# Optimization experiments

Hardware: AMD Instinct MI355X
Metric: run time of the kernel (lower is better)

The kernel has to match this reference:

```python
import jax, jax.numpy as jnp
import numpy as np

N_NODES = 100000
N_EDGES = 600000
VOCAB = 5000
NUM_GRAPHS = 2000
NUM_CLASSES = 10


def setup_inputs() -> dict:
    key = jax.random.key(0)
    ks = jax.random.split(key, 12)
    x = jax.random.randint(ks[0], (N_NODES,), 0, VOCAB, dtype=jnp.int32)
    edge_index = jax.random.randint(ks[1], (2, N_EDGES), 0, N_NODES, dtype=jnp.int32)
    batch = jnp.sort(jax.random.randint(ks[2], (N_NODES,), 0, NUM_GRAPHS, dtype=jnp.int32))
    emb = jax.random.normal(ks[3], (VOCAB, 64), dtype=jnp.float32) * 0.1
    W1 = jax.random.normal(ks[4], (64, 128), dtype=jnp.float32) * (1.0 / np.sqrt(64))
    b1 = jnp.zeros((128,), dtype=jnp.float32)
    W2 = jax.random.normal(ks[5], (128, 128), dtype=jnp.float32) * (1.0 / np.sqrt(128))
    b2 = jnp.zeros((128,), dtype=jnp.float32)
    Wlin = jax.random.normal(ks[6], (128, NUM_CLASSES), dtype=jnp.float32) * (1.0 / np.sqrt(128))
    blin = jnp.zeros((NUM_CLASSES,), dtype=jnp.float32)
    return {"x": x, "edge_index": edge_index, "batch": batch, "num_graphs": NUM_GRAPHS,
            "emb": emb, "W1": W1, "b1": b1, "W2": W2, "b2": b2, "Wlin": Wlin, "blin": blin}


def reference(x, edge_index, batch, num_graphs, emb, W1, b1, W2, b2, Wlin, blin):
    N = x.shape[0]
    loops = jnp.arange(N, dtype=edge_index.dtype)
    src = jnp.concatenate([edge_index[0], loops])  # message sources (j)
    dst = jnp.concatenate([edge_index[1], loops])  # aggregation targets (i)
    # GCN symmetric normalization with self-loops (PyG gcn_norm, source_to_target)
    deg = jax.ops.segment_sum(jnp.ones_like(dst, dtype=jnp.float32), dst, num_segments=N)
    dinv = jnp.where(deg > 0, jax.lax.rsqrt(deg), 0.0)
    norm = dinv[src] * dinv[dst]  # [E+N]

    def gcn(h, W, b):
        h = h @ W  # linear transform first (GCNConv order)
        msg = h[src] * norm[:, None]  # gather + scale, [E+N, F]
        return jax.ops.segment_sum(msg, dst, num_segments=N) + b

    h = emb[x]  # [N, 64]
    h = jax.nn.relu(gcn(h, W1, b1))
    h = jax.nn.relu(gcn(h, W2, b2))
    g = jax.ops.segment_max(h, batch, num_segments=num_graphs)  # global_max_pool
    return g @ Wlin + blin
```

## Files before the change

kernel.cpp:

```cpp
#include <hip/hip_runtime.h>
#include <hip/hip_bf16.h>
#include <hip/hip_fp16.h>


typedef _Float16 h8 __attribute__((ext_vector_type(8)));
typedef float f32x4 __attribute__((ext_vector_type(4)));

__global__ __launch_bounds__(256) void k_zero(int4* __restrict__ deg, int n4i,
                                              int4* __restrict__ pool, int p4i) {
    int t = blockIdx.x * 256 + threadIdx.x;
    int4 z = make_int4(0, 0, 0, 0);
    if (t < n4i) deg[t] = z;
    if (t < p4i) pool[t] = z;
}

__global__ __launch_bounds__(256) void k_degprep(const int* __restrict__ dst, int* __restrict__ deg, int E,
                                                 const float* __restrict__ emb, __half2* __restrict__ e16,
                                                 const float* __restrict__ W1, _Float16* __restrict__ W1T,
                                                 const float* __restrict__ W2, _Float16* __restrict__ W2T,
                                                 int nEmbF, int gE, int nCast) {
    int bid = blockIdx.x;
    if (bid < gE) {
        int e = bid * 256 + threadIdx.x;
        if (e < E) atomicAdd(&deg[dst[e]], 1);
    } else if (bid < gE + nCast) {
        int t = (bid - gE) * 256 + threadIdx.x;
        if (t * 4 < nEmbF) {
            float4 v = *(const float4*)&emb[t * 4];
            e16[t * 2] = __floats2half2_rn(v.x, v.y);
            e16[t * 2 + 1] = __floats2half2_rn(v.z, v.w);
        }
    } else if (bid < gE + nCast + 32) {
        int t = (bid - gE - nCast) * 256 + threadIdx.x;
        int c = t >> 6, k = t & 63;
        W1T[c * 64 + k] = (_Float16)W1[k * 128 + c];
    } else {
        int t = (bid - gE - nCast - 32) * 256 + threadIdx.x;
        if (t < 128 * 128) {
            int c = t >> 7, k = t & 127;
            W2T[c * 128 + k] = (_Float16)W2[k * 128 + c];
        }
    }
}

__global__ __launch_bounds__(256) void k_scan1(const int* __restrict__ deg, int* __restrict__ exc,
                                               int* __restrict__ bsums, float* __restrict__ dinv, int N) {
    __shared__ int s[256];
    int i = blockIdx.x * 256 + threadIdx.x;
    int v = (i < N) ? deg[i] : 0;
    if (i < N) dinv[i] = rsqrtf((float)(v + 1));
    s[threadIdx.x] = v;
    __syncthreads();
    for (int off = 1; off < 256; off <<= 1) {
        int t = (threadIdx.x >= (unsigned)off) ? s[threadIdx.x - off] : 0;
        __syncthreads();
        s[threadIdx.x] += t;
        __syncthreads();
    }
    if (i < N) exc[i] = s[threadIdx.x] - v;
    if (threadIdx.x == 255) bsums[blockIdx.x] = s[255];
}

__global__ __launch_bounds__(512) void k_scan2(int* __restrict__ bsums, int nb) {
    __shared__ int s[512];
    int i = threadIdx.x;
    int v = (i < nb) ? bsums[i] : 0;
    s[i] = v;
    __syncthreads();
    for (int off = 1; off < 512; off <<= 1) {
        int t = (i >= off) ? s[i - off] : 0;
        __syncthreads();
        s[i] += t;
        __syncthreads();
    }
    if (i < nb) bsums[i] = s[i] - v;
}

__global__ __launch_bounds__(256) void k_scan3(int* __restrict__ rowstart, int* __restrict__ cursor,
                                               const int* __restrict__ bsums, int N, int E) {
    int i = blockIdx.x * 256 + threadIdx.x;
    if (i < N) {
        int r = rowstart[i] + bsums[blockIdx.x];
        rowstart[i] = r;
        cursor[i] = r;
    }
    if (i == 0 && blockIdx.x == 0) rowstart[N] = E;
}

__global__ __launch_bounds__(256) void k_fill(const int* __restrict__ src, const int* __restrict__ dst,
                                              const int* __restrict__ x, const float* __restrict__ dinv,
                                              int* __restrict__ cursor, int2* __restrict__ ed,
                                              int* __restrict__ cols, int E) {
    int e = blockIdx.x * 256 + threadIdx.x;
    if (e < E) {
        int d = dst[e];
        int s = src[e];
        int pos = atomicAdd(&cursor[d], 1);
        ed[pos] = make_int2(x[s], __float_as_int(dinv[s]));
        cols[pos] = s;
    }
}

__global__ __launch_bounds__(256) void k_agge(const __half2* __restrict__ e16, const int* __restrict__ x,
                                              const float* __restrict__ dinv, const int* __restrict__ rs,
                                              const int2* __restrict__ ed, __half2* __restrict__ Xagg, int N) {
    int lane = threadIdx.x & 31;
    int n0 = (blockIdx.x * 8 + (threadIdx.x >> 5)) * 2;
    if (n0 >= N) return;
    int nB = (n0 + 1 < N) ? n0 + 1 : n0;
    int cA0 = rs[n0], cA1 = rs[n0 + 1];
    int cB0 = rs[nB], cB1 = rs[nB + 1];
    bool hasA = cA0 < cA1, hasB = cB0 < cB1;
    __half2 tA[8], tB[8];
    float wA[8], wB[8];
    if (hasA) {
#pragma unroll
        for (int i = 0; i < 8; ++i) {
            int ei = cA0 + i;
            int ec = (ei < cA1) ? ei : cA1 - 1;
            int2 r = ed[ec];
            tA[i] = e16[(size_t)r.x * 32 + lane];
            wA[i] = (ei < cA1) ? __int_as_float(r.y) : 0.f;
        }
    }
    if (hasB) {
#pragma unroll
        for (int i = 0; i < 8; ++i) {
            int ei = cB0 + i;
            int ec = (ei < cB1) ? ei : cB1 - 1;
            int2 r = ed[ec];
            tB[i] = e16[(size_t)r.x * 32 + lane];
            wB[i] = (ei < cB1) ? __int_as_float(r.y) : 0.f;
        }
    }
    float dA = dinv[n0], dB = dinv[nB];
    float2 sA = __half22float2(e16[(size_t)x[n0] * 32 + lane]);
    float2 sB = __half22float2(e16[(size_t)x[nB] * 32 + lane]);
    float aA0 = dA * sA.x, aA1 = dA * sA.y;
    float aB0 = dB * sB.x, aB1 = dB * sB.y;
    if (hasA) {
#pragma unroll
        for (int i = 0; i < 8; ++i) {
            float2 tf = __half22float2(tA[i]);
            aA0 = fmaf(wA[i], tf.x, aA0);
            aA1 = fmaf(wA[i], tf.y, aA1);
        }
    }
    if (hasB) {
#pragma unroll
        for (int i = 0; i < 8; ++i) {
            float2 tf = __half22float2(tB[i]);
            aB0 = fmaf(wB[i], tf.x, aB0);
            aB1 = fmaf(wB[i], tf.y, aB1);
        }
    }
    for (int e = cA0 + 8; e < cA1; e += 8) {
#pragma unroll
        for (int i = 0; i < 8; ++i) {
            int ei = e + i;
            int ec = (ei < cA1) ? ei : cA1 - 1;
            int2 r = ed[ec];
            tA[i] = e16[(size_t)r.x * 32 + lane];
            wA[i] = (ei < cA1) ? __int_as_float(r.y) : 0.f;
        }
#pragma unroll
        for (int i = 0; i < 8; ++i) {
            float2 tf = __half22float2(tA[i]);
            aA0 = fmaf(wA[i], tf.x, aA0);
            aA1 = fmaf(wA[i], tf.y, aA1);
        }
    }
    for (int e = cB0 + 8; e < cB1; e += 8) {
#pragma unroll
        for (int i = 0; i < 8; ++i) {
            int ei = e + i;
            int ec = (ei < cB1) ? ei : cB1 - 1;
            int2 r = ed[ec];
            tB[i] = e16[(size_t)r.x * 32 + lane];
            wB[i] = (ei < cB1) ? __int_as_float(r.y) : 0.f;
        }
#pragma unroll
        for (int i = 0; i < 8; ++i) {
            float2 tf = __half22float2(tB[i]);
            aB0 = fmaf(wB[i], tf.x, aB0);
            aB1 = fmaf(wB[i], tf.y, aB1);
        }
    }
    Xagg[(size_t)n0 * 32 + lane] = __floats2half2_rn(dA * aA0, dA * aA1);
    Xagg[(size_t)nB * 32 + lane] = __floats2half2_rn(dB * aB0, dB * aB1);
}

__global__ __launch_bounds__(256) void k_gemm1(const _Float16* __restrict__ A, const _Float16* __restrict__ W1T,
                                               const float* __restrict__ b1, _Float16* __restrict__ h1, int N) {
    int lane = threadIdx.x & 63;
    int wid = threadIdx.x >> 6;
    int r = lane & 15, kg = lane >> 4;
    int row0 = blockIdx.x * 64 + wid * 16;
    int arow = row0 + r;
    if (arow >= N) arow = N - 1;
    const _Float16* ab = A + (size_t)arow * 64 + kg * 8;
    const _Float16* bb = W1T + (size_t)r * 64 + kg * 8;
    f32x4 acc[8];
#pragma unroll
    for (int ct = 0; ct < 8; ++ct) acc[ct] = (f32x4){0.f, 0.f, 0.f, 0.f};
#pragma unroll
    for (int kc = 0; kc < 2; ++kc) {
        h8 a = *(const h8*)(ab + kc * 32);
#pragma unroll
        for (int ct = 0; ct < 8; ++ct) {
            h8 b = *(const h8*)(bb + kc * 32 + ct * 1024);
            acc[ct] = __builtin_amdgcn_mfma_f32_16x16x32_f16(a, b, acc[ct], 0, 0, 0);
        }
    }
#pragma unroll
    for (int ct = 0; ct < 8; ++ct) {
        float bias = b1[ct * 16 + r];
#pragma unroll
        for (int i = 0; i < 4; ++i) {
            int gr = row0 + 4 * kg + i;
            if (gr < N)
                h1[(size_t)gr * 128 + ct * 16 + r] = (_Float16)fmaxf(acc[ct][i] + bias, 0.f);
        }
    }
}

__global__ __launch_bounds__(256) void k_gemm2(const _Float16* __restrict__ A, const _Float16* __restrict__ W2T,
                                               const float* __restrict__ dinv, _Float16* __restrict__ P, int N) {
    int lane = threadIdx.x & 63;
    int wid = threadIdx.x >> 6;
    int r = lane & 15, kg = lane >> 4;
    int row0 = blockIdx.x * 64 + wid * 16;
    int arow = row0 + r;
    if (arow >= N) arow = N - 1;
    const _Float16* ab = A + (size_t)arow * 128 + kg * 8;
    const _Float16* bb = W2T + (size_t)r * 128 + kg * 8;
    f32x4 acc[8];
#pragma unroll
    for (int ct = 0; ct < 8; ++ct) acc[ct] = (f32x4){0.f, 0.f, 0.f, 0.f};
#pragma unroll
    for (int kc = 0; kc < 4; ++kc) {
        h8 a = *(const h8*)(ab + kc * 32);
#pragma unroll
        for (int ct = 0; ct < 8; ++ct) {
            h8 b = *(const h8*)(bb + kc * 32 + ct * 2048);
            acc[ct] = __builtin_amdgcn_mfma_f32_16x16x32_f16(a, b, acc[ct], 0, 0, 0);
        }
    }
    float dv[4];
#pragma unroll
    for (int i = 0; i < 4; ++i) {
        int gr = row0 + 4 * kg + i;
        dv[i] = (gr < N) ? dinv[gr] : 0.f;
    }
#pragma unroll
    for (int ct = 0; ct < 8; ++ct) {
#pragma unroll
        for (int i = 0; i < 4; ++i) {
            int gr = row0 + 4 * kg + i;
            if (gr < N) P[(size_t)gr * 128 + ct * 16 + r] = (_Float16)(acc[ct][i] * dv[i]);
        }
    }
}

typedef _Float16 h4v __attribute__((ext_vector_type(4)));

__global__ __launch_bounds__(512) void k_agg2pool(const h4v* __restrict__ P4, const int* __restrict__ batch,
                                                  const float* __restrict__ dinv, const int* __restrict__ rs,
                                                  const int* __restrict__ cols, const float4* __restrict__ bias4,
                                                  float* __restrict__ pool, int N, int G) {
    __shared__ int lpool[4][128];
    int tid = threadIdx.x;
    lpool[tid >> 7][tid & 127] = 0;
    __syncthreads();
    int lane = tid & 31;
    int blk_n0 = blockIdx.x * 32;
    int gfirst = batch[(blk_n0 < N) ? blk_n0 : (N - 1)];
    int n0 = blk_n0 + (tid >> 5) * 2;
    if (n0 < N) {
        int nB = (n0 + 1 < N) ? n0 + 1 : n0;
        int cA0 = rs[n0], cA1 = rs[n0 + 1];
        int cB0 = rs[nB], cB1 = rs[nB + 1];
        bool hasA = cA0 < cA1, hasB = cB0 < cB1;
        h4v tA[8], tB[8];
        float wA[8], wB[8];
        if (hasA) {
#pragma unroll
            for (int i = 0; i < 8; ++i) {
                int ei = cA0 + i;
                int ec = (ei < cA1) ? ei : cA1 - 1;
                tA[i] = P4[(size_t)cols[ec] * 32 + lane];
                wA[i] = (ei < cA1) ? 1.f : 0.f;
            }
        }
        if (hasB) {
#pragma unroll
            for (int i = 0; i < 8; ++i) {
                int ei = cB0 + i;
                int ec = (ei < cB1) ? ei : cB1 - 1;
                tB[i] = P4[(size_t)cols[ec] * 32 + lane];
                wB[i] = (ei < cB1) ? 1.f : 0.f;
            }
        }
        h4v sA = P4[(size_t)n0 * 32 + lane];
        h4v sB = P4[(size_t)nB * 32 + lane];
        float aA[4], aB[4];
#pragma unroll
        for (int f = 0; f < 4; ++f) {
            aA[f] = (float)sA[f];
            aB[f] = (float)sB[f];
        }
        if (hasA) {
#pragma unroll
            for (int i = 0; i < 8; ++i)
#pragma unroll
                for (int f = 0; f < 4; ++f) aA[f] = fmaf(wA[i], (float)tA[i][f], aA[f]);
        }
        if (hasB) {
#pragma unroll
            for (int i = 0; i < 8; ++i)
#pragma unroll
                for (int f = 0; f < 4; ++f) aB[f] = fmaf(wB[i], (float)tB[i][f], aB[f]);
        }
        for (int e = cA0 + 8; e < cA1; e += 8) {
#pragma unroll
            for (int i = 0; i < 8; ++i) {
                int ei = e + i;
                int ec = (ei < cA1) ? ei : cA1 - 1;
                tA[i] = P4[(size_t)cols[ec] * 32 + lane];
                wA[i] = (ei < cA1) ? 1.f : 0.f;
            }
#pragma unroll
            for (int i = 0; i < 8; ++i)
#pragma unroll
                for (int f = 0; f < 4; ++f) aA[f] = fmaf(wA[i], (float)tA[i][f], aA[f]);
        }
        for (int e = cB0 + 8; e < cB1; e += 8) {
#pragma unroll
            for (int i = 0; i < 8; ++i) {
                int ei = e + i;
                int ec = (ei < cB1) ? ei : cB1 - 1;
                tB[i] = P4[(size_t)cols[ec] * 32 + lane];
                wB[i] = (ei < cB1) ? 1.f : 0.f;
            }
#pragma unroll
            for (int i = 0; i < 8; ++i)
#pragma unroll
                for (int f = 0; f < 4; ++f) aB[f] = fmaf(wB[i], (float)tB[i][f], aB[f]);
        }
        float dA = dinv[n0], dB = dinv[nB];
        int gA = batch[n0], gB = batch[nB];
        float4 b = bias4[lane];
        float bv[4] = {b.x, b.y, b.z, b.w};
        float zA[4], zB[4];
#pragma unroll
        for (int f = 0; f < 4; ++f) {
            zA[f] = fmaxf(fmaf(dA, aA[f], bv[f]), 0.f);
            zB[f] = fmaxf(fmaf(dB, aB[f], bv[f]), 0.f);
        }
        int rot = (lane >> 3) & 3;
        auto emit = [&](int g, const float* m) {
            int slot = g - gfirst;
            if (slot < 4) {
#pragma unroll
                for (int f = 0; f < 4; ++f) {
                    int ff = (f + rot) & 3;
                    if (m[ff] > 0.f) atomicMax(&lpool[slot][lane * 4 + ff], __float_as_int(m[ff]));
                }
            } else {
                float* pg = pool + (size_t)g * 128 + lane * 4;
#pragma unroll
                for (int f = 0; f < 4; ++f)
                    if (m[f] > 0.f) atomicMax((int*)(pg + f), __float_as_int(m[f]));
            }
        };
        if (gA == gB) {
            float m[4];
#pragma unroll
            for (int f = 0; f < 4; ++f) m[f] = fmaxf(zA[f], zB[f]);
            emit(gA, m);
        } else {
            emit(gA, zA);
            emit(gB, zB);
        }
    }
    __syncthreads();
    int s = tid >> 7, f = tid & 127;
    int v = lpool[s][f];
    if (v > 0) atomicMax((int*)&pool[(size_t)(gfirst + s) * 128 + f], v);
}

__global__ __launch_bounds__(256) void k_final(const float* __restrict__ pool, const float* __restrict__ Wlin,
                                               const float* __restrict__ blin, float* __restrict__ out, int G) {
    int t = blockIdx.x * 256 + threadIdx.x;
    if (t >= G * 10) return;
    int g = t / 10, c = t % 10;
    float acc = blin[c];
    const float* pr = pool + (size_t)g * 128;
#pragma unroll 8
    for (int f = 0; f < 128; ++f) acc = fmaf(pr[f], Wlin[f * 10 + c], acc);
    out[t] = acc;
}

extern "C" void kernel_launch(void* const* d_in, const int* in_sizes, int n_in,
                              void* d_out, int out_size, void* d_ws, size_t ws_size,
                              hipStream_t stream) {
    const int* x = (const int*)d_in[0];
    const int* ei = (const int*)d_in[1];
    const int* batch = (const int*)d_in[2];
    const float* emb = (const float*)d_in[4];
    const float* W1 = (const float*)d_in[5];
    const float* b1 = (const float*)d_in[6];
    const float* W2 = (const float*)d_in[7];
    const float* b2 = (const float*)d_in[8];
    const float* Wlin = (const float*)d_in[9];
    const float* blin = (const float*)d_in[10];
    float* out = (float*)d_out;

    int N = in_sizes[0];
    int E = in_sizes[1] / 2;
    int VOCAB = in_sizes[4] / 64;
    int G = out_size / 10;
    const int* srcp = ei;
    const int* dstp = ei + E;

    char* p = (char*)d_ws;
    auto alloc = [&](size_t bytes) -> char* {
        char* r = p;
        p += (bytes + 255) & ~(size_t)255;
        return r;
    };
    int* deg = (int*)alloc((size_t)N * 4);
    int* cursor = (int*)alloc((size_t)N * 4);
    int* rowstart = (int*)alloc((size_t)(N + 1) * 4);
    int* bsums = (int*)alloc(512 * 4);
    float* dinv = (float*)alloc((size_t)N * 4);
    int2* ed = (int2*)alloc((size_t)E * 8);
    int* cols = (int*)alloc((size_t)E * 4);
    _Float16* e16 = (_Float16*)alloc((size_t)VOCAB * 64 * 2);
    _Float16* W1T = (_Float16*)alloc(128 * 64 * 2);
    _Float16* W2T = (_Float16*)alloc(128 * 128 * 2);
    _Float16* Xagg = (_Float16*)alloc((size_t)N * 64 * 2);
    _Float16* h1 = (_Float16*)alloc((size_t)N * 128 * 2);
    _Float16* P = (_Float16*)alloc((size_t)N * 128 * 2);
    float* pool = (float*)alloc((size_t)G * 128 * 4);

    int gE = (E + 255) / 256;
    int gN = (N + 255) / 256;
    int nEmbF = VOCAB * 64;
    int nCast = (nEmbF / 4 + 255) / 256;

    int n4i = N / 4, p4i = G * 128 / 4;
    int zg = ((n4i > p4i ? n4i : p4i) + 255) / 256;
    k_zero<<<zg, 256, 0, stream>>>((int4*)deg, n4i, (int4*)pool, p4i);
    k_degprep<<<gE + nCast + 32 + 64, 256, 0, stream>>>(dstp, deg, E, emb, (__half2*)e16, W1, W1T,
                                                        W2, W2T, nEmbF, gE, nCast);
    k_scan1<<<gN, 256, 0, stream>>>(deg, rowstart, bsums, dinv, N);
    k_scan2<<<1, 512, 0, stream>>>(bsums, gN);
    k_scan3<<<gN, 256, 0, stream>>>(rowstart, cursor, bsums, N, E);
    k_fill<<<gE, 256, 0, stream>>>(srcp, dstp, x, dinv, cursor, ed, cols, E);
    k_agge<<<(N + 15) / 16, 256, 0, stream>>>((const __half2*)e16, x, dinv, rowstart, ed,
                                              (__half2*)Xagg, N);
    k_gemm1<<<(N + 63) / 64, 256, 0, stream>>>(Xagg, W1T, b1, h1, N);
    k_gemm2<<<(N + 63) / 64, 256, 0, stream>>>(h1, W2T, dinv, P, N);
    k_agg2pool<<<(N + 31) / 32, 512, 0, stream>>>((const h4v*)P, batch, dinv, rowstart, cols,
                                                  (const float4*)b2, pool, N, G);
    k_final<<<(G * 10 + 255) / 256, 256, 0, stream>>>(pool, Wlin, blin, out, G);
}
```

Measured before the change: 214.0 us.

## Fuse layer-1 aggregation and both GEMMs into one kernel; widen agg2pool gather batch

Merges the embedding aggregation, GEMM1 (with bias+ReLU) and GEMM2 (scaled by dinv) into a single kernel per 64-node tile. The intermediate Xagg and h1 now live in shared memory instead of global buffers, which removes two global round-trips and two launches. The layer-2 aggregation+pool kernel now uses 256-thread blocks covering 16 nodes and issues 16 gathers per node in flight instead of 8, to raise memory-level parallelism. The trade-offs are higher register pressure and more wasted loads for low-degree nodes.

```diff
diff --git a/kernel.cpp b/kernel.cpp
--- a/kernel.cpp
+++ b/kernel.cpp
@@ -4,6 +4,7 @@
 
 
 typedef _Float16 h8 __attribute__((ext_vector_type(8)));
+typedef _Float16 h4v __attribute__((ext_vector_type(4)));
 typedef float f32x4 __attribute__((ext_vector_type(4)));
 
 __global__ __launch_bounds__(256) void k_zero(int4* __restrict__ deg, int n4i,
@@ -101,207 +102,171 @@
     }
 }
 
-__global__ __launch_bounds__(256) void k_agge(const __half2* __restrict__ e16, const int* __restrict__ x,
-                                              const float* __restrict__ dinv, const int* __restrict__ rs,
-                                              const int2* __restrict__ ed, __half2* __restrict__ Xagg, int N) {
-    int lane = threadIdx.x & 31;
-    int n0 = (blockIdx.x * 8 + (threadIdx.x >> 5)) * 2;
-    if (n0 >= N) return;
-    int nB = (n0 + 1 < N) ? n0 + 1 : n0;
-    int cA0 = rs[n0], cA1 = rs[n0 + 1];
-    int cB0 = rs[nB], cB1 = rs[nB + 1];
-    bool hasA = cA0 < cA1, hasB = cB0 < cB1;
-    __half2 tA[8], tB[8];
-    float wA[8], wB[8];
-    if (hasA) {
-#pragma unroll
-        for (int i = 0; i < 8; ++i) {
-            int ei = cA0 + i;
-            int ec = (ei < cA1) ? ei : cA1 - 1;
-            int2 r = ed[ec];
-            tA[i] = e16[(size_t)r.x * 32 + lane];
-            wA[i] = (ei < cA1) ? __int_as_float(r.y) : 0.f;
-        }
-    }
-    if (hasB) {
-#pragma unroll
-        for (int i = 0; i < 8; ++i) {
-            int ei = cB0 + i;
-            int ec = (ei < cB1) ? ei : cB1 - 1;
-            int2 r = ed[ec];
-            tB[i] = e16[(size_t)r.x * 32 + lane];
-            wB[i] = (ei < cB1) ? __int_as_float(r.y) : 0.f;
-        }
-    }
-    float dA = dinv[n0], dB = dinv[nB];
-    float2 sA = __half22float2(e16[(size_t)x[n0] * 32 + lane]);
-    float2 sB = __half22float2(e16[(size_t)x[nB] * 32 + lane]);
-    float aA0 = dA * sA.x, aA1 = dA * sA.y;
-    float aB0 = dB * sB.x, aB1 = dB * sB.y;
-    if (hasA) {
-#pragma unroll
-        for (int i = 0; i < 8; ++i) {
-            float2 tf = __half22float2(tA[i]);
-            aA0 = fmaf(wA[i], tf.x, aA0);
-            aA1 = fmaf(wA[i], tf.y, aA1);
-        }
-    }
-    if (hasB) {
-#pragma unroll
-        for (int i = 0; i < 8; ++i) {
-            float2 tf = __half22float2(tB[i]);
-            aB0 = fmaf(wB[i], tf.x, aB0);
-            aB1 = fmaf(wB[i], tf.y, aB1);
-        }
-    }
-    for (int e = cA0 + 8; e < cA1; e += 8) {
-#pragma unroll
-        for (int i = 0; i < 8; ++i) {
-            int ei = e + i;
-            int ec = (ei < cA1) ? ei : cA1 - 1;
-            int2 r = ed[ec];
-            tA[i] = e16[(size_t)r.x * 32 + lane];
-            wA[i] = (ei < cA1) ? __int_as_float(r.y) : 0.f;
-        }
-#pragma unroll
-        for (int i = 0; i < 8; ++i) {
-            float2 tf = __half22float2(tA[i]);
-            aA0 = fmaf(wA[i], tf.x, aA0);
-            aA1 = fmaf(wA[i], tf.y, aA1);
-        }
-    }
-    for (int e = cB0 + 8; e < cB1; e += 8) {
-#pragma unroll
-        for (int i = 0; i < 8; ++i) {
-            int ei = e + i;
-            int ec = (ei < cB1) ? ei : cB1 - 1;
-            int2 r = ed[ec];
-            tB[i] = e16[(size_t)r.x * 32 + lane];
-            wB[i] = (ei < cB1) ? __int_as_float(r.y) : 0.f;
-        }
-#pragma unroll
-        for (int i = 0; i < 8; ++i) {
-            float2 tf = __half22float2(tB[i]);
-            aB0 = fmaf(wB[i], tf.x, aB0);
-            aB1 = fmaf(wB[i], tf.y, aB1);
-        }
-    }
-    Xagg[(size_t)n0 * 32 + lane] = __floats2half2_rn(dA * aA0, dA * aA1);
-    Xagg[(size_t)nB * 32 + lane] = __floats2half2_rn(dB * aB0, dB * aB1);
-}
-
-__global__ __launch_bounds__(256) void k_gemm1(const _Float16* __restrict__ A, const _Float16* __restrict__ W1T,
-                                               const float* __restrict__ b1, _Float16* __restrict__ h1, int N) {
-    int lane = threadIdx.x & 63;
-    int wid = threadIdx.x >> 6;
-    int r = lane & 15, kg = lane >> 4;
-    int row0 = blockIdx.x * 64 + wid * 16;
-    int arow = row0 + r;
-    if (arow >= N) arow = N - 1;
-    const _Float16* ab = A + (size_t)arow * 64 + kg * 8;
-    const _Float16* bb = W1T + (size_t)r * 64 + kg * 8;
-    f32x4 acc[8];
-#pragma unroll
-    for (int ct = 0; ct < 8; ++ct) acc[ct] = (f32x4){0.f, 0.f, 0.f, 0.f};
-#pragma unroll
-    for (int kc = 0; kc < 2; ++kc) {
-        h8 a = *(const h8*)(ab + kc * 32);
+__global__ __launch_bounds__(256) void k_mlp(const __half2* __restrict__ e16, const int* __restrict__ x,
+                                             const float* __restrict__ dinv, const int* __restrict__ rs,
+                                             const int2* __restrict__ ed, const _Float16* __restrict__ W1T,
+                                             const float* __restrict__ b1, const _Float16* __restrict__ W2T,
+                                             _Float16* __restrict__ P, int N) {
+    __shared__ _Float16 Xs[64][72];
+    __shared__ _Float16 Hs[64][136];
+    int tid = threadIdx.x;
+    int blk0 = blockIdx.x * 64;
+    {
+        int lane = tid & 31;
+        int hw = tid >> 5;
+        for (int pass = 0; pass < 4; ++pass) {
+            int nl = hw * 8 + pass * 2;
+            int gA = blk0 + nl;     if (gA >= N) gA = N - 1;
+            int gB = blk0 + nl + 1; if (gB >= N) gB = N - 1;
+            int cA0 = rs[gA], cA1 = rs[gA + 1];
+            int cB0 = rs[gB], cB1 = rs[gB + 1];
+            bool hasA = cA0 < cA1, hasB = cB0 < cB1;
+            __half2 tA[8], tB[8];
+            float wA[8], wB[8];
+#pragma unroll
+            for (int i = 0; i < 8; ++i) {
+                int ei = cA0 + i;
+                int ec = (ei < cA1) ? ei : (hasA ? cA1 - 1 : 0);
+                int2 r2 = ed[ec];
+                tA[i] = e16[(size_t)r2.x * 32 + lane];
+                wA[i] = (ei < cA1) ? __int_as_float(r2.y) : 0.f;
+            }
+#pragma unroll
+            for (int i = 0; i < 8; ++i) {
+                int ei = cB0 + i;
+                int ec = (ei < cB1) ? ei : (hasB ? cB1 - 1 : 0);
+                int2 r2 = ed[ec];
+                tB[i] = e16[(size_t)r2.x * 32 + lane];
+                wB[i] = (ei < cB1) ? __int_as_float(r2.y) : 0.f;
+            }
+            float dA = dinv[gA], dB = dinv[gB];
+            float2 sA = __half22float2(e16[(size_t)x[gA] * 32 + lane]);
+            float2 sB = __half22float2(e16[(size_t)x[gB] * 32 + lane]);
+            float aA0 = dA * sA.x, aA1 = dA * sA.y;
+            float aB0 = dB * sB.x, aB1 = dB * sB.y;
+#pragma unroll
+            for (int i = 0; i < 8; ++i) {
+                float2 tf = __half22float2(tA[i]);
+                aA0 = fmaf(wA[i], tf.x, aA0);
+                aA1 = fmaf(wA[i], tf.y, aA1);
+            }
+#pragma unroll
+            for (int i = 0; i < 8; ++i) {
+                float2 tf = __half22float2(tB[i]);
+                aB0 = fmaf(wB[i], tf.x, aB0);
+                aB1 = fmaf(wB[i], tf.y, aB1);
+            }
+            for (int e = cA0 + 8; e < cA1; e += 8) {
+#pragma unroll
+                for (int i = 0; i < 8; ++i) {
+                    int ei = e + i;
+                    int ec = (ei < cA1) ? ei : cA1 - 1;
+                    int2 r2 = ed[ec];
+                    tA[i] = e16[(size_t)r2.x * 32 + lane];
+                    wA[i] = (ei < cA1) ? __int_as_float(r2.y) : 0.f;
+                }
+#pragma unroll
+                for (int i = 0; i < 8; ++i) {
+                    float2 tf = __half22float2(tA[i]);
+                    aA0 = fmaf(wA[i], tf.x, aA0);
+                    aA1 = fmaf(wA[i], tf.y, aA1);
+                }
+            }
+            for (int e = cB0 + 8; e < cB1; e += 8) {
+#pragma unroll
+                for (int i = 0; i < 8; ++i) {
+                    int ei = e + i;
+                    int ec = (ei < cB1) ? ei : cB1 - 1;
+                    int2 r2 = ed[ec];
+                    tB[i] = e16[(size_t)r2.x * 32 + lane];
+                    wB[i] = (ei < cB1) ? __int_as_float(r2.y) : 0.f;
+                }
+#pragma unroll
+                for (int i = 0; i < 8; ++i) {
+                    float2 tf = __half22float2(tB[i]);
+                    aB0 = fmaf(wB[i], tf.x, aB0);
+                    aB1 = fmaf(wB[i], tf.y, aB1);
+                }
+            }
+            *(__half2*)&Xs[nl][lane * 2] = __floats2half2_rn(dA * aA0, dA * aA1);
+            *(__half2*)&Xs[nl + 1][lane * 2] = __floats2half2_rn(dB * aB0, dB * aB1);
+        }
+    }
+    __syncthreads();
+    int l = tid & 63, wid = tid >> 6;
+    int r = l & 15, kg = l >> 4;
+    {
+        f32x4 acc[8];
+#pragma unroll
+        for (int ct = 0; ct < 8; ++ct) acc[ct] = (f32x4){0.f, 0.f, 0.f, 0.f};
+#pragma unroll
+        for (int kc = 0; kc < 2; ++kc) {
+            h8 a = *(const h8*)&Xs[wid * 16 + r][kc * 32 + kg * 8];
+#pragma unroll
+            for (int ct = 0; ct < 8; ++ct) {
+                h8 b = *(const h8*)(W1T + (size_t)r * 64 + kg * 8 + kc * 32 + ct * 1024);
+                acc[ct] = __builtin_amdgcn_mfma_f32_16x16x32_f16(a, b, acc[ct], 0, 0, 0);
+            }
+        }
 #pragma unroll
         for (int ct = 0; ct < 8; ++ct) {
-            h8 b = *(const h8*)(bb + kc * 32 + ct * 1024);
-            acc[ct] = __builtin_amdgcn_mfma_f32_16x16x32_f16(a, b, acc[ct], 0, 0, 0);
-        }
-    }
-#pragma unroll
-    for (int ct = 0; ct < 8; ++ct) {
-        float bias = b1[ct * 16 + r];
+            float bias = b1[ct * 16 + r];
+#pragma unroll
+            for (int i = 0; i < 4; ++i)
+                Hs[wid * 16 + 4 * kg + i][ct * 16 + r] = (_Float16)fmaxf(acc[ct][i] + bias, 0.f);
+        }
+    }
+    __syncthreads();
+    {
+        f32x4 acc[8];
+#pragma unroll
+        for (int ct = 0; ct < 8; ++ct) acc[ct] = (f32x4){0.f, 0.f, 0.f, 0.f};
+#pragma unroll
+        for (int kc = 0; kc < 4; ++kc) {
+            h8 a = *(const h8*)&Hs[wid * 16 + r][kc * 32 + kg * 8];
+#pragma unroll
+            for (int ct = 0; ct < 8; ++ct) {
+                h8 b = *(const h8*)(W2T + (size_t)r * 128 + kg * 8 + kc * 32 + ct * 2048);
+                acc[ct] = __builtin_amdgcn_mfma_f32_16x16x32_f16(a, b, acc[ct], 0, 0, 0);
+            }
+        }
+        float dv[4];
 #pragma unroll
         for (int i = 0; i < 4; ++i) {
-            int gr = row0 + 4 * kg + i;
-            if (gr < N)
-                h1[(size_t)gr * 128 + ct * 16 + r] = (_Float16)fmaxf(acc[ct][i] + bias, 0.f);
-        }
-    }
-}
-
-__global__ __launch_bounds__(256) void k_gemm2(const _Float16* __restrict__ A, const _Float16* __restrict__ W2T,
-                                               const float* __restrict__ dinv, _Float16* __restrict__ P, int N) {
-    int lane = threadIdx.x & 63;
-    int wid = threadIdx.x >> 6;
-    int r = lane & 15, kg = lane >> 4;
-    int row0 = blockIdx.x * 64 + wid * 16;
-    int arow = row0 + r;
-    if (arow >= N) arow = N - 1;
-    const _Float16* ab = A + (size_t)arow * 128 + kg * 8;
-    const _Float16* bb = W2T + (size_t)r * 128 + kg * 8;
-    f32x4 acc[8];
-#pragma unroll
-    for (int ct = 0; ct < 8; ++ct) acc[ct] = (f32x4){0.f, 0.f, 0.f, 0.f};
-#pragma unroll
-    for (int kc = 0; kc < 4; ++kc) {
-        h8 a = *(const h8*)(ab + kc * 32);
+            int gr = blk0 + wid * 16 + 4 * kg + i;
+            dv[i] = (gr < N) ? dinv[gr] : 0.f;
+        }
 #pragma unroll
         for (int ct = 0; ct < 8; ++ct) {
-            h8 b = *(const h8*)(bb + kc * 32 + ct * 2048);
-            acc[ct] = __builtin_amdgcn_mfma_f32_16x16x32_f16(a, b, acc[ct], 0, 0, 0);
-        }
-    }
-    float dv[4];
-#pragma unroll
-    for (int i = 0; i < 4; ++i) {
-        int gr = row0 + 4 * kg + i;
-        dv[i] = (gr < N) ? dinv[gr] : 0.f;
-    }
-#pragma unroll
-    for (int ct = 0; ct < 8; ++ct) {
-#pragma unroll
-        for (int i = 0; i < 4; ++i) {
-            int gr = row0 + 4 * kg + i;
-            if (gr < N) P[(size_t)gr * 128 + ct * 16 + r] = (_Float16)(acc[ct][i] * dv[i]);
-        }
-    }
-}
-
-typedef _Float16 h4v __attribute__((ext_vector_type(4)));
-
-__global__ __launch_bounds__(512) void k_agg2pool(const h4v* __restrict__ P4, const int* __restrict__ batch,
+#pragma unroll
+            for (int i = 0; i < 4; ++i) {
+                int gr = blk0 + wid * 16 + 4 * kg + i;
+                if (gr < N) P[(size_t)gr * 128 + ct * 16 + r] = (_Float16)(acc[ct][i] * dv[i]);
+            }
+        }
+    }
+}
+
+__global__ __launch_bounds__(256) void k_agg2pool(const h4v* __restrict__ P4, const int* __restrict__ batch,
                                                   const float* __restrict__ dinv, const int* __restrict__ rs,
                                                   const int* __restrict__ cols, const float4* __restrict__ bias4,
                                                   float* __restrict__ pool, int N, int G) {
     __shared__ int lpool[4][128];
     int tid = threadIdx.x;
     lpool[tid >> 7][tid & 127] = 0;
+    lpool[(tid >> 7) + 2][tid & 127] = 0;
     __syncthreads();
     int lane = tid & 31;
-    int blk_n0 = blockIdx.x * 32;
+    int blk_n0 = blockIdx.x * 16;
     int gfirst = batch[(blk_n0 < N) ? blk_n0 : (N - 1)];
     int n0 = blk_n0 + (tid >> 5) * 2;
     if (n0 < N) {
+        int nA = n0;
         int nB = (n0 + 1 < N) ? n0 + 1 : n0;
-        int cA0 = rs[n0], cA1 = rs[n0 + 1];
+        int cA0 = rs[nA], cA1 = rs[nA + 1];
         int cB0 = rs[nB], cB1 = rs[nB + 1];
         bool hasA = cA0 < cA1, hasB = cB0 < cB1;
-        h4v tA[8], tB[8];
-        float wA[8], wB[8];
-        if (hasA) {
-#pragma unroll
-            for (int i = 0; i < 8; ++i) {
-                int ei = cA0 + i;
-                int ec = (ei < cA1) ? ei : cA1 - 1;
-                tA[i] = P4[(size_t)cols[ec] * 32 + lane];
-                wA[i] = (ei < cA1) ? 1.f : 0.f;
-            }
-        }
-        if (hasB) {
-#pragma unroll
-            for (int i = 0; i < 8; ++i) {
-                int ei = cB0 + i;
-                int ec = (ei < cB1) ? ei : cB1 - 1;
-                tB[i] = P4[(size_t)cols[ec] * 32 + lane];
-                wB[i] = (ei < cB1) ? 1.f : 0.f;
-            }
-        }
-        h4v sA = P4[(size_t)n0 * 32 + lane];
+        h4v sA = P4[(size_t)nA * 32 + lane];
         h4v sB = P4[(size_t)nB * 32 + lane];
         float aA[4], aB[4];
 #pragma unroll
@@ -309,46 +274,65 @@
             aA[f] = (float)sA[f];
             aB[f] = (float)sB[f];
         }
-        if (hasA) {
-#pragma unroll
-            for (int i = 0; i < 8; ++i)
-#pragma unroll
-                for (int f = 0; f < 4; ++f) aA[f] = fmaf(wA[i], (float)tA[i][f], aA[f]);
-        }
-        if (hasB) {
-#pragma unroll
-            for (int i = 0; i < 8; ++i)
-#pragma unroll
-                for (int f = 0; f < 4; ++f) aB[f] = fmaf(wB[i], (float)tB[i][f], aB[f]);
-        }
-        for (int e = cA0 + 8; e < cA1; e += 8) {
-#pragma unroll
-            for (int i = 0; i < 8; ++i) {
+        {
+            h4v tA[16], tB[16];
+#pragma unroll
+            for (int i = 0; i < 16; ++i) {
+                int ei = cA0 + i;
+                int ec = (ei < cA1) ? ei : (hasA ? cA1 - 1 : 0);
+                tA[i] = P4[(size_t)cols[ec] * 32 + lane];
+            }
+#pragma unroll
+            for (int i = 0; i < 16; ++i) {
+                int ei = cB0 + i;
+                int ec = (ei < cB1) ? ei : (hasB ? cB1 - 1 : 0);
+                tB[i] = P4[(size_t)cols[ec] * 32 + lane];
+            }
+#pragma unroll
+            for (int i = 0; i < 16; ++i) {
+                float w = (cA0 + i < cA1) ? 1.f : 0.f;
+#pragma unroll
+                for (int f = 0; f < 4; ++f) aA[f] = fmaf(w, (float)tA[i][f], aA[f]);
+            }
+#pragma unroll
+            for (int i = 0; i < 16; ++i) {
+                float w = (cB0 + i < cB1) ? 1.f : 0.f;
+#pragma unroll
+                for (int f = 0; f < 4; ++f) aB[f] = fmaf(w, (float)tB[i][f], aB[f]);
+            }
+        }
+        for (int e = cA0 + 16; e < cA1; e += 16) {
+            h4v t[16];
+#pragma unroll
+            for (int i = 0; i < 16; ++i) {
                 int ei = e + i;
                 int ec = (ei < cA1) ? ei : cA1 - 1;
-                tA[i] = P4[(size_t)cols[ec] * 32 + lane];
-                wA[i] = (ei < cA1) ? 1.f : 0.f;
-            }
-#pragma unroll
-            for (int i = 0; i < 8; ++i)
-#pragma unroll
-                for (int f = 0; f < 4; ++f) aA[f] = fmaf(wA[i], (float)tA[i][f], aA[f]);
-        }
-        for (int e = cB0 + 8; e < cB1; e += 8) {
-#pragma unroll
-            for (int i = 0; i < 8; ++i) {
+                t[i] = P4[(size_t)cols[ec] * 32 + lane];
+            }
+#pragma unroll
+            for (int i = 0; i < 16; ++i) {
+                float w = (e + i < cA1) ? 1.f : 0.f;
+#pragma unroll
+                for (int f = 0; f < 4; ++f) aA[f] = fmaf(w, (float)t[i][f], aA[f]);
+            }
+        }
+        for (int e = cB0 + 16; e < cB1; e += 16) {
+            h4v t[16];
+#pragma unroll
+            for (int i = 0; i < 16; ++i) {
                 int ei = e + i;
                 int ec = (ei < cB1) ? ei : cB1 - 1;
-                tB[i] = P4[(size_t)cols[ec] * 32 + lane];
-                wB[i] = (ei < cB1) ? 1.f : 0.f;
-            }
-#pragma unroll
-            for (int i = 0; i < 8; ++i)
-#pragma unroll
-                for (int f = 0; f < 4; ++f) aB[f] = fmaf(wB[i], (float)tB[i][f], aB[f]);
-        }
-        float dA = dinv[n0], dB = dinv[nB];
-        int gA = batch[n0], gB = batch[nB];
+                t[i] = P4[(size_t)cols[ec] * 32 + lane];
+            }
+#pragma unroll
+            for (int i = 0; i < 16; ++i) {
+                float w = (e + i < cB1) ? 1.f : 0.f;
+#pragma unroll
+                for (int f = 0; f < 4; ++f) aB[f] = fmaf(w, (float)t[i][f], aB[f]);
+            }
+        }
+        float dA = dinv[nA], dB = dinv[nB];
+        int gA = batch[nA], gB = batch[nB];
         float4 b = bias4[lane];
         float bv[4] = {b.x, b.y, b.z, b.w};
         float zA[4], zB[4];
@@ -384,9 +368,13 @@
         }
     }
     __syncthreads();
-    int s = tid >> 7, f = tid & 127;
-    int v = lpool[s][f];
-    if (v > 0) atomicMax((int*)&pool[(size_t)(gfirst + s) * 128 + f], v);
+    {
+        int f = tid & 127;
+        for (int s = tid >> 7; s < 4; s += 2) {
+            int v = lpool[s][f];
+            if (v > 0) atomicMax((int*)&pool[(size_t)(gfirst + s) * 128 + f], v);
+        }
+    }
 }
 
 __global__ __launch_bounds__(256) void k_final(const float* __restrict__ pool, const float* __restrict__ Wlin,
@@ -439,8 +427,6 @@
     _Float16* e16 = (_Float16*)alloc((size_t)VOCAB * 64 * 2);
     _Float16* W1T = (_Float16*)alloc(128 * 64 * 2);
     _Float16* W2T = (_Float16*)alloc(128 * 128 * 2);
-    _Float16* Xagg = (_Float16*)alloc((size_t)N * 64 * 2);
-    _Float16* h1 = (_Float16*)alloc((size_t)N * 128 * 2);
     _Float16* P = (_Float16*)alloc((size_t)N * 128 * 2);
     float* pool = (float*)alloc((size_t)G * 128 * 4);
 
@@ -458,11 +444,9 @@
     k_scan2<<<1, 512, 0, stream>>>(bsums, gN);
     k_scan3<<<gN, 256, 0, stream>>>(rowstart, cursor, bsums, N, E);
     k_fill<<<gE, 256, 0, stream>>>(srcp, dstp, x, dinv, cursor, ed, cols, E);
-    k_agge<<<(N + 15) / 16, 256, 0, stream>>>((const __half2*)e16, x, dinv, rowstart, ed,
-                                              (__half2*)Xagg, N);
-    k_gemm1<<<(N + 63) / 64, 256, 0, stream>>>(Xagg, W1T, b1, h1, N);
-    k_gemm2<<<(N + 63) / 64, 256, 0, stream>>>(h1, W2T, dinv, P, N);
-    k_agg2pool<<<(N + 31) / 32, 512, 0, stream>>>((const h4v*)P, batch, dinv, rowstart, cols,
+    k_mlp<<<(N + 63) / 64, 256, 0, stream>>>((const __half2*)e16, x, dinv, rowstart, ed, W1T, b1,
+                                             W2T, P, N);
+    k_agg2pool<<<(N + 15) / 16, 256, 0, stream>>>((const h4v*)P, batch, dinv, rowstart, cols,
                                                   (const float4*)b2, pool, N, G);
     k_final<<<(G * 10 + 255) / 256, 256, 0, stream>>>(pool, Wlin, blin, out, G);
 }
```

New measurement: 196.5 us. -8.2%, faster.
